# Kernel tuning notes

Measured on AMD Instinct MI355X. Metric: run time of the kernel, lower is better.

Reference implementation:

```python
import jax, jax.numpy as jnp
import numpy as np

S, L, D = 128, 512, 256   # MSA rows, residues, msa_dim
H, C = 8, 32              # num_heads, head_dim


def setup_inputs() -> dict:
    key = jax.random.key(0)
    ks = jax.random.split(key, 8)
    inp = {
        "msa_input": jax.random.normal(ks[0], (S, L, D), dtype=jnp.float32),
        "ln_scale": jnp.ones((D,), jnp.float32),
        "ln_bias": jnp.zeros((D,), jnp.float32),
        "wq": jax.random.normal(ks[1], (D, H * C), jnp.float32) / np.sqrt(D),
        "wk": jax.random.normal(ks[2], (D, H * C), jnp.float32) / np.sqrt(D),
        "wv": jax.random.normal(ks[3], (D, H * C), jnp.float32) / np.sqrt(D),
        "wg": jax.random.normal(ks[4], (D, H * C), jnp.float32) / np.sqrt(D),
        "bg": jnp.zeros((H * C,), jnp.float32),
        "wo": jax.random.normal(ks[5], (H * C, D), jnp.float32) / np.sqrt(H * C),
        "bo": jnp.zeros((D,), jnp.float32),
    }
    return inp


def reference(msa_input, ln_scale, ln_bias, wq, wk, wv, wg, bg, wo, bo):
    # LayerNorm over last dim (eps matches torch default 1e-5)
    mu = jnp.mean(msa_input, axis=-1, keepdims=True)
    var = jnp.mean(jnp.square(msa_input - mu), axis=-1, keepdims=True)
    x = (msa_input - mu) * jax.lax.rsqrt(var + 1e-5) * ln_scale + ln_bias

    q = (x @ wq).reshape(S, L, H, C)
    k = (x @ wk).reshape(S, L, H, C)
    v = (x @ wv).reshape(S, L, H, C)
    g = jax.nn.sigmoid(x @ wg + bg).reshape(S, L, H, C)

    scale = 1.0 / np.sqrt(C)
    # attention over MSA-row axis, per residue l and head h
    scores = jnp.einsum("slhc,tlhc->stlh", q, k) * scale   # [S,S,L,H]
    probs = jax.nn.softmax(scores, axis=1)                  # softmax over t
    o = jnp.einsum("stlh,tlhc->slhc", probs, v) * g         # [S,L,H,C]
    return o.reshape(S, L, H * C) @ wo + bo
```

## Files before the change

### kernel.cpp

```cpp
#include <hip/hip_runtime.h>
#include <hip/hip_bf16.h>

typedef __bf16 bf16;
typedef __bf16 bf16x8 __attribute__((ext_vector_type(8)));
typedef float f32x4 __attribute__((ext_vector_type(4)));

#define S_DIM 128
#define L_DIM 512
#define D_DIM 256
#define NQ    1024

__device__ __forceinline__ void gl16(void* lds, const void* g) {
  __builtin_amdgcn_global_load_lds((const __attribute__((address_space(1))) void*)g,
                                   (__attribute__((address_space(3))) void*)lds,
                                   16, 0, 0);
}

__global__ void pack_weights(const float* __restrict__ wq, const float* __restrict__ wk,
                             const float* __restrict__ wv, const float* __restrict__ wg,
                             const float* __restrict__ wo,
                             bf16* __restrict__ wcat_t, bf16* __restrict__ wo_t) {
  int idx = blockIdx.x * 256 + threadIdx.x;
  const int total1 = NQ * D_DIM;
  if (idx < total1) {
    int j = idx >> 8;
    int d = idx & 255;
    const float* w = (j < 256) ? wq : (j < 512) ? wk : (j < 768) ? wv : wg;
    wcat_t[idx] = (bf16)w[d * 256 + (j & 255)];
  } else {
    int i2 = idx - total1;
    if (i2 < D_DIM * D_DIM) {
      int dcol = i2 >> 8, k = i2 & 255;
      wo_t[i2] = (bf16)wo[k * 256 + dcol];
    }
  }
}

__global__ __launch_bounds__(256) void ln_kernel(const float* __restrict__ x,
                                                 const float* __restrict__ sc,
                                                 const float* __restrict__ bs,
                                                 bf16* __restrict__ y) {
  int wid  = threadIdx.x >> 6;
  int lane = threadIdx.x & 63;
  int row  = blockIdx.x * 4 + wid;
  float4 v = ((const float4*)(x + (size_t)row * D_DIM))[lane];
  float s = v.x + v.y + v.z + v.w;
  #pragma unroll
  for (int m = 32; m; m >>= 1) s += __shfl_xor(s, m);
  float mu = s * (1.0f / 256.0f);
  float dx = v.x - mu, dy = v.y - mu, dz = v.z - mu, dw = v.w - mu;
  float s2 = dx * dx + dy * dy + dz * dz + dw * dw;
  #pragma unroll
  for (int m = 32; m; m >>= 1) s2 += __shfl_xor(s2, m);
  float rs = rsqrtf(s2 * (1.0f / 256.0f) + 1e-5f);
  float4 scv = ((const float4*)sc)[lane];
  float4 bsv = ((const float4*)bs)[lane];
  union { uint2 u; bf16 b[4]; } o;
  o.b[0] = (bf16)(dx * rs * scv.x + bsv.x);
  o.b[1] = (bf16)(dy * rs * scv.y + bsv.y);
  o.b[2] = (bf16)(dz * rs * scv.z + bsv.z);
  o.b[3] = (bf16)(dw * rs * scv.w + bsv.w);
  ((uint2*)y)[(size_t)row * 64 + lane] = o.u;
}

__device__ __forceinline__ bf16x8 lds_swz(const bf16* base, int row, int k) {
  return *(const bf16x8*)((const char*)base + ((((row << 6) + k) << 1) ^ ((row & 7) << 4)));
}

__global__ __launch_bounds__(256, 4) void gemm_qkvg(const bf16* __restrict__ A,
                                                    const bf16* __restrict__ Bt,
                                                    bf16* __restrict__ Cout,
                                                    const float* __restrict__ bias) {
  __shared__ __align__(16) bf16 smem[16384];
  bf16* As = smem;
  bf16* Bs = smem + 8192;
  const int tid  = threadIdx.x;
  const int wid  = tid >> 6;
  const int lane = tid & 63;
  const int bid   = blockIdx.x;
  const int n_idx = (bid >> 3) & 7;
  const int m_idx = (bid & 7) | ((bid >> 6) << 3);
  const int m0 = m_idx * 128;
  const int n0 = n_idx * 128;
  const int lrow = lane & 15;
  const int lk   = (lane >> 4) * 8;
  const int wr = wid >> 1, wc = wid & 1;

  const int ln8 = lane >> 3;
  const int c8  = ((lane & 7) ^ ln8) * 8;

  const bf16* Arow = A  + (size_t)m0 * 256 + c8;
  const bf16* Brow = Bt + (size_t)n0 * 256 + c8;

  f32x4 acc[4][4] = {};

  #pragma unroll
  for (int ks = 0; ks < 4; ++ks) {
    const int k0 = ks * 64;
    #pragma unroll
    for (int t = 0; t < 4; ++t) {
      int chunk = wid * 4 + t;
      int r = chunk * 8 + ln8;
      gl16(&As[chunk * 512], Arow + (size_t)r * 256 + k0);
      gl16(&Bs[chunk * 512], Brow + (size_t)r * 256 + k0);
    }
    __syncthreads();
    #pragma unroll
    for (int kk = 0; kk < 64; kk += 32) {
      bf16x8 av[4], bv[4];
      #pragma unroll
      for (int i = 0; i < 4; ++i)
        av[i] = lds_swz(As, wr * 64 + i * 16 + lrow, kk + lk);
      #pragma unroll
      for (int j = 0; j < 4; ++j)
        bv[j] = lds_swz(Bs, wc * 64 + j * 16 + lrow, kk + lk);
      #pragma unroll
      for (int i = 0; i < 4; ++i)
        #pragma unroll
        for (int j = 0; j < 4; ++j)
          acc[i][j] = __builtin_amdgcn_mfma_f32_16x16x32_bf16(av[i], bv[j], acc[i][j], 0, 0, 0);
    }
    __syncthreads();
  }

  const int rb = (lane >> 4) * 4;
  const int xorv = rb << 2;

  const bool isg = (n0 >= 768);
  float bgv[4];
  if (isg) {
    #pragma unroll
    for (int j = 0; j < 4; ++j) bgv[j] = bias[n0 - 768 + wc * 64 + j * 16 + lrow];
  }
  #pragma unroll
  for (int i = 0; i < 4; ++i)
    #pragma unroll
    for (int j = 0; j < 4; ++j) {
      int col = wc * 64 + j * 16 + lrow;
      #pragma unroll
      for (int r = 0; r < 4; ++r) {
        int row = wr * 64 + i * 16 + rb + r;
        float v = acc[i][j][r];
        if (isg) { v += bgv[j]; v = 1.0f / (1.0f + __expf(-v)); }
        smem[row * 128 + (col ^ xorv)] = (bf16)v;
      }
    }
  __syncthreads();
  #pragma unroll
  for (int p = 0; p < 8; ++p) {
    int chunk = p * 256 + tid;
    int row = chunk >> 4, slot8 = (chunk & 15) * 8;
    int rx = (row & 12) << 2;
    *(uint4*)(Cout + (size_t)(m0 + row) * NQ + n0 + slot8) =
        *(const uint4*)(smem + row * 128 + (slot8 ^ rx));
  }
}

__global__ __launch_bounds__(512) void attn_proj(const bf16* __restrict__ qkvg,
                                                 const bf16* __restrict__ wo_t,
                                                 const float* __restrict__ bo,
                                                 float* __restrict__ out) {
  __shared__ __align__(16) char smem[155648];
  const int tid  = threadIdx.x;
  const int wid  = tid >> 6;
  const int lane = tid & 63;
  const int lrow = lane & 15;
  const int lkg  = lane >> 4;
  const int lk   = lkg * 8;
  const int rb   = lkg * 4;
  const int res  = blockIdx.x;
  const int hc0  = wid * 32;

  bf16* vw = (bf16*)smem + wid * (32 * 136);
  bf16* pw = (bf16*)(smem + 69632) + wid * (16 * 72);
  bf16* of = (bf16*)(smem + 88064);

  {
    int t0 = lane >> 2, cs = (lane & 3) * 8;
    #pragma unroll
    for (int pass = 0; pass < 8; ++pass) {
      int t = pass * 16 + t0;
      union { uint4 u; bf16 e[8]; } v;
      v.u = *(const uint4*)(qkvg + (size_t)(t * L_DIM + res) * NQ + 512 + hc0 + cs);
      #pragma unroll
      for (int j = 0; j < 8; ++j) vw[(cs + j) * 136 + t] = v.e[j];
    }
  }

  bf16x8 kf[8];
  #pragma unroll
  for (int tt = 0; tt < 8; ++tt)
    kf[tt] = *(const bf16x8*)(qkvg + (size_t)((tt * 16 + lrow) * L_DIM + res) * NQ + 256 + hc0 + lk);

  const float scale = 0.17677669529663687f;
  const f32x4 z = {0.f, 0.f, 0.f, 0.f};

  for (int st = 0; st < 8; ++st) {
    bf16x8 qf = *(const bf16x8*)(qkvg + (size_t)((st * 16 + lrow) * L_DIM + res) * NQ + hc0 + lk);
    f32x4 sc[8];
    #pragma unroll
    for (int tt = 0; tt < 8; ++tt)
      sc[tt] = __builtin_amdgcn_mfma_f32_16x16x32_bf16(qf, kf[tt], z, 0, 0, 0);

    #pragma unroll
    for (int r = 0; r < 4; ++r) {
      float m = sc[0][r];
      #pragma unroll
      for (int tc = 1; tc < 8; ++tc) m = fmaxf(m, sc[tc][r]);
      #pragma unroll
      for (int msk = 8; msk; msk >>= 1) m = fmaxf(m, __shfl_xor(m, msk));
      float pv[8], ssum = 0.f;
      #pragma unroll
      for (int tc = 0; tc < 8; ++tc) {
        float p = __expf((sc[tc][r] - m) * scale);
        pv[tc] = p; ssum += p;
      }
      #pragma unroll
      for (int msk = 8; msk; msk >>= 1) ssum += __shfl_xor(ssum, msk);
      float inv = 1.0f / ssum;
      #pragma unroll
      for (int tc = 0; tc < 8; ++tc) sc[tc][r] = pv[tc] * inv;
    }

    f32x4 oc[2] = {z, z};
    #pragma unroll
    for (int hf = 0; hf < 2; ++hf) {
      #pragma unroll
      for (int tc = 0; tc < 4; ++tc)
        #pragma unroll
        for (int r = 0; r < 4; ++r)
          pw[(rb + r) * 72 + tc * 16 + lrow] = (bf16)sc[hf * 4 + tc][r];
      #pragma unroll
      for (int kc = 0; kc < 2; ++kc) {
        bf16x8 pa = *(const bf16x8*)(pw + lrow * 72 + kc * 32 + lk);
        #pragma unroll
        for (int ct = 0; ct < 2; ++ct) {
          bf16x8 bv = *(const bf16x8*)(vw + (ct * 16 + lrow) * 136 + hf * 64 + kc * 32 + lk);
          oc[ct] = __builtin_amdgcn_mfma_f32_16x16x32_bf16(pa, bv, oc[ct], 0, 0, 0);
        }
      }
    }
    #pragma unroll
    for (int ct = 0; ct < 2; ++ct)
      #pragma unroll
      for (int r = 0; r < 4; ++r)
        of[(st * 16 + rb + r) * 264 + hc0 + ct * 16 + lrow] = (bf16)oc[ct][r];
  }
  __syncthreads();

  const int pbase = (wid >> 1) * 32;
  const int pn    = wid & 1;

  bf16x8 af[2][8];
  #pragma unroll
  for (int mt = 0; mt < 2; ++mt) {
    int s = pbase + mt * 16 + lrow;
    #pragma unroll
    for (int kt = 0; kt < 8; ++kt) {
      bf16x8 o8 = *(const bf16x8*)(of + s * 264 + kt * 32 + lk);
      bf16x8 g8 = *(const bf16x8*)(qkvg + (size_t)(s * L_DIM + res) * NQ + 768 + kt * 32 + lk);
      bf16x8 rr;
      #pragma unroll
      for (int j = 0; j < 8; ++j) rr[j] = (bf16)((float)o8[j] * (float)g8[j]);
      af[mt][kt] = rr;
    }
  }

  float bov[2][4];
  #pragma unroll
  for (int hf = 0; hf < 2; ++hf)
    #pragma unroll
    for (int nt = 0; nt < 4; ++nt)
      bov[hf][nt] = bo[hf * 128 + pn * 64 + nt * 16 + lrow];

  bf16* wS = (bf16*)smem;
  f32x4 acc[2][2][4] = {};
  #pragma unroll
  for (int hf = 0; hf < 2; ++hf) {
    #pragma unroll
    for (int pass = 0; pass < 8; ++pass) {
      int ch = pass * 512 + tid;
      int dl = ch >> 5, sl = ch & 31;
      gl16((char*)wS + (pass * 512 + wid * 64) * 16,
           wo_t + (size_t)(hf * 128 + dl) * 256 + (sl ^ (dl & 7)) * 8);
    }
    __syncthreads();
    #pragma unroll
    for (int kt = 0; kt < 8; ++kt)
      #pragma unroll
      for (int nt = 0; nt < 4; ++nt) {
        int dl = pn * 64 + nt * 16 + lrow;
        bf16x8 bw = *(const bf16x8*)((char*)wS + dl * 512 + (((kt * 4 + lkg) ^ (dl & 7)) * 16));
        acc[hf][0][nt] = __builtin_amdgcn_mfma_f32_16x16x32_bf16(af[0][kt], bw, acc[hf][0][nt], 0, 0, 0);
        acc[hf][1][nt] = __builtin_amdgcn_mfma_f32_16x16x32_bf16(af[1][kt], bw, acc[hf][1][nt], 0, 0, 0);
      }
    __syncthreads();
  }

  float* fb = (float*)smem;
  #pragma unroll 1
  for (int b = 0; b < 4; ++b) {
    if ((wid >> 1) == b) {
      #pragma unroll
      for (int hf = 0; hf < 2; ++hf)
        #pragma unroll
        for (int mt = 0; mt < 2; ++mt)
          #pragma unroll
          for (int nt = 0; nt < 4; ++nt)
            #pragma unroll
            for (int r = 0; r < 4; ++r)
              fb[(mt * 16 + rb + r) * 264 + hf * 128 + pn * 64 + nt * 16 + lrow] =
                  acc[hf][mt][nt][r] + bov[hf][nt];
    }
    __syncthreads();
    #pragma unroll
    for (int u = 0; u < 4; ++u) {
      int ch = u * 512 + tid;
      int row = ch >> 6, c4 = (ch & 63) * 4;
      *(uint4*)(out + (size_t)((b * 32 + row) * L_DIM + res) * 256 + c4) =
          *(const uint4*)(fb + row * 264 + c4);
    }
    __syncthreads();
  }
}

extern "C" void kernel_launch(void* const* d_in, const int* in_sizes, int n_in,
                              void* d_out, int out_size, void* d_ws, size_t ws_size,
                              hipStream_t stream) {
  const float* msa      = (const float*)d_in[0];
  const float* ln_scale = (const float*)d_in[1];
  const float* ln_bias  = (const float*)d_in[2];
  const float* wq       = (const float*)d_in[3];
  const float* wk       = (const float*)d_in[4];
  const float* wv       = (const float*)d_in[5];
  const float* wg       = (const float*)d_in[6];
  const float* bg       = (const float*)d_in[7];
  const float* wo       = (const float*)d_in[8];
  const float* bo       = (const float*)d_in[9];
  float* out = (float*)d_out;

  char* ws = (char*)d_ws;
  bf16* wcat_t = (bf16*)ws;
  bf16* wo_t   = (bf16*)(ws + 524288);
  bf16* qkvg   = (bf16*)(ws + 655360);
  bf16* x_ln   = (bf16*)d_out;

  pack_weights<<<dim3(1280), dim3(256), 0, stream>>>(wq, wk, wv, wg, wo, wcat_t, wo_t);
  ln_kernel<<<dim3(65536 / 4), dim3(256), 0, stream>>>(msa, ln_scale, ln_bias, x_ln);
  gemm_qkvg<<<dim3(4096), dim3(256), 0, stream>>>(x_ln, wcat_t, qkvg, bg);
  attn_proj<<<dim3(512), dim3(512), 0, stream>>>(qkvg, wo_t, bo, out);
}
```

Measured before the change: 156.9 us.

## Repack QKVG into per-residue head-pair panels and split attention from output projection

The QKVG GEMM now writes its output as contiguous per-(type, residue, head-pair) panels, so the attention loads are contiguous instead of strided by L*NQ. The fused attention+projection kernel becomes two kernels: a smaller attention kernel (256 threads, two blocks per residue, gating applied in-loop) that writes a bf16 gated output buffer, and a separate tiled GEMM for the output projection. This is meant to fix uncoalesced attention loads and the large-LDS, low-occupancy fused kernel. The cost is an extra global round-trip of the gated output and one more launch.

New measurement: 156.1 us. About the same (-0.5%).

```diff
diff --git a/kernel.cpp b/kernel.cpp
--- a/kernel.cpp
+++ b/kernel.cpp
@@ -69,7 +69,7 @@
 
 __global__ __launch_bounds__(256, 4) void gemm_qkvg(const bf16* __restrict__ A,
                                                     const bf16* __restrict__ Bt,
-                                                    bf16* __restrict__ Cout,
+                                                    bf16* __restrict__ pan,
                                                     const float* __restrict__ bias) {
   __shared__ __align__(16) bf16 smem[16384];
   bf16* As = smem;
@@ -126,11 +126,11 @@
   const int rb = (lane >> 4) * 4;
   const int xorv = rb << 2;
 
-  const bool isg = (n0 >= 768);
+  const bool isg = (n_idx >= 6);
   float bgv[4];
   if (isg) {
     #pragma unroll
-    for (int j = 0; j < 4; ++j) bgv[j] = bias[n0 - 768 + wc * 64 + j * 16 + lrow];
+    for (int j = 0; j < 4; ++j) bgv[j] = bias[(n_idx & 1) * 128 + wc * 64 + j * 16 + lrow];
   }
   #pragma unroll
   for (int i = 0; i < 4; ++i)
@@ -146,21 +146,24 @@
       }
     }
   __syncthreads();
+
+  const int type = n_idx >> 1;
+  const int hp0  = (n_idx & 1) * 2;
+  const int s    = m_idx >> 2;
+  const int res0 = (m_idx & 3) * 128;
   #pragma unroll
   for (int p = 0; p < 8; ++p) {
-    int chunk = p * 256 + tid;
-    int row = chunk >> 4, slot8 = (chunk & 15) * 8;
-    int rx = (row & 12) << 2;
-    *(uint4*)(Cout + (size_t)(m0 + row) * NQ + n0 + slot8) =
-        *(const uint4*)(smem + row * 128 + (slot8 ^ rx));
-  }
-}
-
-__global__ __launch_bounds__(512) void attn_proj(const bf16* __restrict__ qkvg,
-                                                 const bf16* __restrict__ wo_t,
-                                                 const float* __restrict__ bo,
-                                                 float* __restrict__ out) {
-  __shared__ __align__(16) char smem[155648];
+    int ch = p * 256 + tid;
+    int c16 = ch & 7, hpl = (ch >> 3) & 1, rr = ch >> 4;
+    int col = hpl * 64 + c16 * 8;
+    *(uint4*)(pan + ((size_t)((type * 512 + res0 + rr) * 4) + hp0 + hpl) * 8192 + s * 64 + c16 * 8) =
+        *(const uint4*)(smem + rr * 128 + (col ^ ((rr & 12) << 2)));
+  }
+}
+
+__global__ __launch_bounds__(256, 3) void attn_kernel(const bf16* __restrict__ pan,
+                                                      bf16* __restrict__ obuf) {
+  __shared__ __align__(16) char smem[48640];
   const int tid  = threadIdx.x;
   const int wid  = tid >> 6;
   const int lane = tid & 63;
@@ -168,20 +171,29 @@
   const int lkg  = lane >> 4;
   const int lk   = lkg * 8;
   const int rb   = lkg * 4;
-  const int res  = blockIdx.x;
-  const int hc0  = wid * 32;
-
-  bf16* vw = (bf16*)smem + wid * (32 * 136);
-  bf16* pw = (bf16*)(smem + 69632) + wid * (16 * 72);
-  bf16* of = (bf16*)(smem + 88064);
+  const int bid  = blockIdx.x;
+  const int res  = bid >> 1;
+  const int hg   = bid & 1;
+  const int h    = hg * 4 + wid;
+  const int hp   = h >> 1;
+  const int hl   = (h & 1) * 32;
+
+  bf16* vw  = (bf16*)smem + wid * (32 * 136);
+  bf16* pwb = (bf16*)(smem + 34816) + wid * (16 * 72);
+  bf16* osb = (bf16*)(smem + 44032) + wid * (16 * 36);
+
+  const bf16* Pq = pan + ((size_t)((0 * 512 + res) * 4) + hp) * 8192 + hl;
+  const bf16* Pk = pan + ((size_t)((1 * 512 + res) * 4) + hp) * 8192 + hl;
+  const bf16* Pv = pan + ((size_t)((2 * 512 + res) * 4) + hp) * 8192 + hl;
+  const bf16* Pg = pan + ((size_t)((3 * 512 + res) * 4) + hp) * 8192 + hl;
 
   {
     int t0 = lane >> 2, cs = (lane & 3) * 8;
     #pragma unroll
-    for (int pass = 0; pass < 8; ++pass) {
-      int t = pass * 16 + t0;
+    for (int p = 0; p < 8; ++p) {
+      int t = p * 16 + t0;
       union { uint4 u; bf16 e[8]; } v;
-      v.u = *(const uint4*)(qkvg + (size_t)(t * L_DIM + res) * NQ + 512 + hc0 + cs);
+      v.u = *(const uint4*)(Pv + t * 64 + cs);
       #pragma unroll
       for (int j = 0; j < 8; ++j) vw[(cs + j) * 136 + t] = v.e[j];
     }
@@ -190,13 +202,13 @@
   bf16x8 kf[8];
   #pragma unroll
   for (int tt = 0; tt < 8; ++tt)
-    kf[tt] = *(const bf16x8*)(qkvg + (size_t)((tt * 16 + lrow) * L_DIM + res) * NQ + 256 + hc0 + lk);
+    kf[tt] = *(const bf16x8*)(Pk + (tt * 16 + lrow) * 64 + lk);
 
   const float scale = 0.17677669529663687f;
   const f32x4 z = {0.f, 0.f, 0.f, 0.f};
 
   for (int st = 0; st < 8; ++st) {
-    bf16x8 qf = *(const bf16x8*)(qkvg + (size_t)((st * 16 + lrow) * L_DIM + res) * NQ + hc0 + lk);
+    bf16x8 qf = *(const bf16x8*)(Pq + (st * 16 + lrow) * 64 + lk);
     f32x4 sc[8];
     #pragma unroll
     for (int tt = 0; tt < 8; ++tt)
@@ -229,10 +241,10 @@
       for (int tc = 0; tc < 4; ++tc)
         #pragma unroll
         for (int r = 0; r < 4; ++r)
-          pw[(rb + r) * 72 + tc * 16 + lrow] = (bf16)sc[hf * 4 + tc][r];
+          pwb[(rb + r) * 72 + tc * 16 + lrow] = (bf16)sc[hf * 4 + tc][r];
       #pragma unroll
       for (int kc = 0; kc < 2; ++kc) {
-        bf16x8 pa = *(const bf16x8*)(pw + lrow * 72 + kc * 32 + lk);
+        bf16x8 pa = *(const bf16x8*)(pwb + lrow * 72 + kc * 32 + lk);
         #pragma unroll
         for (int ct = 0; ct < 2; ++ct) {
           bf16x8 bv = *(const bf16x8*)(vw + (ct * 16 + lrow) * 136 + hf * 64 + kc * 32 + lk);
@@ -244,83 +256,107 @@
     for (int ct = 0; ct < 2; ++ct)
       #pragma unroll
       for (int r = 0; r < 4; ++r)
-        of[(st * 16 + rb + r) * 264 + hc0 + ct * 16 + lrow] = (bf16)oc[ct][r];
-  }
-  __syncthreads();
-
-  const int pbase = (wid >> 1) * 32;
-  const int pn    = wid & 1;
-
-  bf16x8 af[2][8];
-  #pragma unroll
-  for (int mt = 0; mt < 2; ++mt) {
-    int s = pbase + mt * 16 + lrow;
-    #pragma unroll
-    for (int kt = 0; kt < 8; ++kt) {
-      bf16x8 o8 = *(const bf16x8*)(of + s * 264 + kt * 32 + lk);
-      bf16x8 g8 = *(const bf16x8*)(qkvg + (size_t)(s * L_DIM + res) * NQ + 768 + kt * 32 + lk);
-      bf16x8 rr;
-      #pragma unroll
-      for (int j = 0; j < 8; ++j) rr[j] = (bf16)((float)o8[j] * (float)g8[j]);
-      af[mt][kt] = rr;
-    }
-  }
-
-  float bov[2][4];
-  #pragma unroll
-  for (int hf = 0; hf < 2; ++hf)
-    #pragma unroll
-    for (int nt = 0; nt < 4; ++nt)
-      bov[hf][nt] = bo[hf * 128 + pn * 64 + nt * 16 + lrow];
-
-  bf16* wS = (bf16*)smem;
-  f32x4 acc[2][2][4] = {};
-  #pragma unroll
-  for (int hf = 0; hf < 2; ++hf) {
-    #pragma unroll
-    for (int pass = 0; pass < 8; ++pass) {
-      int ch = pass * 512 + tid;
-      int dl = ch >> 5, sl = ch & 31;
-      gl16((char*)wS + (pass * 512 + wid * 64) * 16,
-           wo_t + (size_t)(hf * 128 + dl) * 256 + (sl ^ (dl & 7)) * 8);
-    }
-    __syncthreads();
-    #pragma unroll
-    for (int kt = 0; kt < 8; ++kt)
-      #pragma unroll
-      for (int nt = 0; nt < 4; ++nt) {
-        int dl = pn * 64 + nt * 16 + lrow;
-        bf16x8 bw = *(const bf16x8*)((char*)wS + dl * 512 + (((kt * 4 + lkg) ^ (dl & 7)) * 16));
-        acc[hf][0][nt] = __builtin_amdgcn_mfma_f32_16x16x32_bf16(af[0][kt], bw, acc[hf][0][nt], 0, 0, 0);
-        acc[hf][1][nt] = __builtin_amdgcn_mfma_f32_16x16x32_bf16(af[1][kt], bw, acc[hf][1][nt], 0, 0, 0);
+        osb[(rb + r) * 36 + ct * 16 + lrow] = (bf16)oc[ct][r];
+    {
+      int row = lane >> 2, c16 = (lane & 3) * 8;
+      bf16x8 o8 = *(const bf16x8*)(osb + row * 36 + c16);
+      bf16x8 g8 = *(const bf16x8*)(Pg + (st * 16 + row) * 64 + c16);
+      bf16x8 r8;
+      #pragma unroll
+      for (int u = 0; u < 8; ++u) r8[u] = (bf16)((float)o8[u] * (float)g8[u]);
+      *(uint4*)(obuf + ((size_t)res * 128 + st * 16 + row) * 256 + h * 32 + c16) = *(uint4*)&r8;
+    }
+  }
+}
+
+__global__ __launch_bounds__(256, 4) void gemm_proj(const bf16* __restrict__ A,
+                                                    const bf16* __restrict__ Bt,
+                                                    float* __restrict__ Cout,
+                                                    const float* __restrict__ bias) {
+  __shared__ __align__(16) bf16 smem[16384];
+  bf16* As = smem;
+  bf16* Bs = smem + 8192;
+  const int tid  = threadIdx.x;
+  const int wid  = tid >> 6;
+  const int lane = tid & 63;
+  const int bid   = blockIdx.x;
+  const int n_idx = (bid >> 3) & 1;
+  const int m_idx = (bid & 7) | ((bid >> 4) << 3);
+  const int m0 = m_idx * 128;
+  const int n0 = n_idx * 128;
+  const int lrow = lane & 15;
+  const int lk   = (lane >> 4) * 8;
+  const int wr = wid >> 1, wc = wid & 1;
+
+  const int ln8 = lane >> 3;
+  const int c8  = ((lane & 7) ^ ln8) * 8;
+
+  const bf16* Arow = A  + (size_t)m0 * 256 + c8;
+  const bf16* Brow = Bt + (size_t)n0 * 256 + c8;
+
+  f32x4 acc[4][4] = {};
+
+  #pragma unroll
+  for (int ks = 0; ks < 4; ++ks) {
+    const int k0 = ks * 64;
+    #pragma unroll
+    for (int t = 0; t < 4; ++t) {
+      int chunk = wid * 4 + t;
+      int r = chunk * 8 + ln8;
+      gl16(&As[chunk * 512], Arow + (size_t)r * 256 + k0);
+      gl16(&Bs[chunk * 512], Brow + (size_t)r * 256 + k0);
+    }
+    __syncthreads();
+    #pragma unroll
+    for (int kk = 0; kk < 64; kk += 32) {
+      bf16x8 av[4], bv[4];
+      #pragma unroll
+      for (int i = 0; i < 4; ++i)
+        av[i] = lds_swz(As, wr * 64 + i * 16 + lrow, kk + lk);
+      #pragma unroll
+      for (int j = 0; j < 4; ++j)
+        bv[j] = lds_swz(Bs, wc * 64 + j * 16 + lrow, kk + lk);
+      #pragma unroll
+      for (int i = 0; i < 4; ++i)
+        #pragma unroll
+        for (int j = 0; j < 4; ++j)
+          acc[i][j] = __builtin_amdgcn_mfma_f32_16x16x32_bf16(av[i], bv[j], acc[i][j], 0, 0, 0);
+    }
+    __syncthreads();
+  }
+
+  const int rb = (lane >> 4) * 4;
+  const int xorv = rb << 2;
+  float* smf = (float*)smem;
+  float bov[4];
+  #pragma unroll
+  for (int j = 0; j < 4; ++j) bov[j] = bias[n0 + wc * 64 + j * 16 + lrow];
+  #pragma unroll
+  for (int half = 0; half < 2; ++half) {
+    if (half) __syncthreads();
+    #pragma unroll
+    for (int i2 = 0; i2 < 2; ++i2) {
+      int i = half * 2 + i2;
+      #pragma unroll
+      for (int j = 0; j < 4; ++j) {
+        int col = wc * 64 + j * 16 + lrow;
+        #pragma unroll
+        for (int r = 0; r < 4; ++r) {
+          int crow = wr * 32 + i2 * 16 + rb + r;
+          smf[crow * 128 + (col ^ xorv)] = acc[i][j][r] + bov[j];
+        }
       }
-    __syncthreads();
-  }
-
-  float* fb = (float*)smem;
-  #pragma unroll 1
-  for (int b = 0; b < 4; ++b) {
-    if ((wid >> 1) == b) {
-      #pragma unroll
-      for (int hf = 0; hf < 2; ++hf)
-        #pragma unroll
-        for (int mt = 0; mt < 2; ++mt)
-          #pragma unroll
-          for (int nt = 0; nt < 4; ++nt)
-            #pragma unroll
-            for (int r = 0; r < 4; ++r)
-              fb[(mt * 16 + rb + r) * 264 + hf * 128 + pn * 64 + nt * 16 + lrow] =
-                  acc[hf][mt][nt][r] + bov[hf][nt];
-    }
-    __syncthreads();
-    #pragma unroll
-    for (int u = 0; u < 4; ++u) {
-      int ch = u * 512 + tid;
-      int row = ch >> 6, c4 = (ch & 63) * 4;
-      *(uint4*)(out + (size_t)((b * 32 + row) * L_DIM + res) * 256 + c4) =
-          *(const uint4*)(fb + row * 264 + c4);
-    }
-    __syncthreads();
+    }
+    __syncthreads();
+    #pragma unroll
+    for (int p = 0; p < 8; ++p) {
+      int ch = p * 256 + tid;
+      int crow = ch >> 5, slot = (ch & 31) * 4;
+      int rx = (crow & 12) << 2;
+      int s_loc = (crow >> 5) * 64 + half * 32 + (crow & 31);
+      *(uint4*)(Cout + ((size_t)s_loc * 512 + m_idx) * 256 + n0 + slot) =
+          *(const uint4*)(smf + crow * 128 + (slot ^ rx));
+    }
   }
 }
 
@@ -342,11 +378,13 @@
   char* ws = (char*)d_ws;
   bf16* wcat_t = (bf16*)ws;
   bf16* wo_t   = (bf16*)(ws + 524288);
-  bf16* qkvg   = (bf16*)(ws + 655360);
+  bf16* pan    = (bf16*)(ws + 655360);
+  bf16* obuf   = (bf16*)(ws + 655360 + 134217728ULL);
   bf16* x_ln   = (bf16*)d_out;
 
   pack_weights<<<dim3(1280), dim3(256), 0, stream>>>(wq, wk, wv, wg, wo, wcat_t, wo_t);
   ln_kernel<<<dim3(65536 / 4), dim3(256), 0, stream>>>(msa, ln_scale, ln_bias, x_ln);
-  gemm_qkvg<<<dim3(4096), dim3(256), 0, stream>>>(x_ln, wcat_t, qkvg, bg);
-  attn_proj<<<dim3(512), dim3(512), 0, stream>>>(qkvg, wo_t, bo, out);
-}
+  gemm_qkvg<<<dim3(4096), dim3(256), 0, stream>>>(x_ln, wcat_t, pan, bg);
+  attn_kernel<<<dim3(1024), dim3(256), 0, stream>>>(pan, obuf);
+  gemm_proj<<<dim3(1024), dim3(256), 0, stream>>>(obuf, wo_t, out, bo);
+}
```

## Fuse LayerNorm into QKVG projection per residue and write head-panel layout

Applied to the files above, without the earlier changes.

Merges the LayerNorm and QKVG GEMM kernels into one per-residue kernel. It normalizes all 128 MSA rows into LDS, streams the concatenated weights in double-buffered 64-column chunks, and writes Q/K/V/G into a per-residue, per-head-pair panel layout. The attention kernel then reads contiguous panels instead of rows strided by L. This removes the bf16 LN round trip through global memory and one launch. In exchange it uses only 512 blocks with large LDS, and each block re-reads the full weight matrix.

After: 154.2 us. About the same (-1.7%).

```diff
diff --git a/kernel.cpp b/kernel.cpp
--- a/kernel.cpp
+++ b/kernel.cpp
@@ -36,130 +36,147 @@
   }
 }
 
-__global__ __launch_bounds__(256) void ln_kernel(const float* __restrict__ x,
-                                                 const float* __restrict__ sc,
-                                                 const float* __restrict__ bs,
-                                                 bf16* __restrict__ y) {
-  int wid  = threadIdx.x >> 6;
-  int lane = threadIdx.x & 63;
-  int row  = blockIdx.x * 4 + wid;
-  float4 v = ((const float4*)(x + (size_t)row * D_DIM))[lane];
-  float s = v.x + v.y + v.z + v.w;
-  #pragma unroll
-  for (int m = 32; m; m >>= 1) s += __shfl_xor(s, m);
-  float mu = s * (1.0f / 256.0f);
-  float dx = v.x - mu, dy = v.y - mu, dz = v.z - mu, dw = v.w - mu;
-  float s2 = dx * dx + dy * dy + dz * dz + dw * dw;
-  #pragma unroll
-  for (int m = 32; m; m >>= 1) s2 += __shfl_xor(s2, m);
-  float rs = rsqrtf(s2 * (1.0f / 256.0f) + 1e-5f);
-  float4 scv = ((const float4*)sc)[lane];
-  float4 bsv = ((const float4*)bs)[lane];
-  union { uint2 u; bf16 b[4]; } o;
-  o.b[0] = (bf16)(dx * rs * scv.x + bsv.x);
-  o.b[1] = (bf16)(dy * rs * scv.y + bsv.y);
-  o.b[2] = (bf16)(dz * rs * scv.z + bsv.z);
-  o.b[3] = (bf16)(dw * rs * scv.w + bsv.w);
-  ((uint2*)y)[(size_t)row * 64 + lane] = o.u;
-}
-
-__device__ __forceinline__ bf16x8 lds_swz(const bf16* base, int row, int k) {
-  return *(const bf16x8*)((const char*)base + ((((row << 6) + k) << 1) ^ ((row & 7) << 4)));
-}
-
-__global__ __launch_bounds__(256, 4) void gemm_qkvg(const bf16* __restrict__ A,
-                                                    const bf16* __restrict__ Bt,
-                                                    bf16* __restrict__ Cout,
-                                                    const float* __restrict__ bias) {
-  __shared__ __align__(16) bf16 smem[16384];
-  bf16* As = smem;
-  bf16* Bs = smem + 8192;
+__global__ __launch_bounds__(512, 2) void ln_qkvg(const float* __restrict__ msa,
+                                                  const float* __restrict__ lns,
+                                                  const float* __restrict__ lnb,
+                                                  const bf16* __restrict__ wcat,
+                                                  const float* __restrict__ bg,
+                                                  bf16* __restrict__ pan) {
+  __shared__ __align__(16) char smem[147456];
+  bf16* Albs = (bf16*)smem;
+  char* Bb   = smem + 65536;
+  bf16* Cst  = (bf16*)(smem + 131072);
   const int tid  = threadIdx.x;
   const int wid  = tid >> 6;
   const int lane = tid & 63;
-  const int bid   = blockIdx.x;
-  const int n_idx = (bid >> 3) & 7;
-  const int m_idx = (bid & 7) | ((bid >> 6) << 3);
-  const int m0 = m_idx * 128;
-  const int n0 = n_idx * 128;
   const int lrow = lane & 15;
-  const int lk   = (lane >> 4) * 8;
-  const int wr = wid >> 1, wc = wid & 1;
-
-  const int ln8 = lane >> 3;
-  const int c8  = ((lane & 7) ^ ln8) * 8;
-
-  const bf16* Arow = A  + (size_t)m0 * 256 + c8;
-  const bf16* Brow = Bt + (size_t)n0 * 256 + c8;
-
-  f32x4 acc[4][4] = {};
-
-  #pragma unroll
-  for (int ks = 0; ks < 4; ++ks) {
-    const int k0 = ks * 64;
-    #pragma unroll
-    for (int t = 0; t < 4; ++t) {
-      int chunk = wid * 4 + t;
-      int r = chunk * 8 + ln8;
-      gl16(&As[chunk * 512], Arow + (size_t)r * 256 + k0);
-      gl16(&Bs[chunk * 512], Brow + (size_t)r * 256 + k0);
-    }
-    __syncthreads();
-    #pragma unroll
-    for (int kk = 0; kk < 64; kk += 32) {
-      bf16x8 av[4], bv[4];
+  const int lkg  = lane >> 4;
+  const int lk   = lkg * 8;
+  const int rb   = lkg * 4;
+  const int res  = blockIdx.x;
+
+  #pragma unroll
+  for (int p = 0; p < 4; ++p) {
+    int ch = p * 512 + tid;
+    int n = ch >> 5;
+    int inner = (ch & 31) * 16;
+    gl16(Bb + p * 8192 + wid * 1024,
+         (const char*)wcat + (size_t)n * 512 + (inner ^ ((n & 7) << 4)));
+  }
+
+  {
+    float4 scv = ((const float4*)lns)[lane];
+    float4 bsv = ((const float4*)lnb)[lane];
+    const float* mbase = msa + ((size_t)(wid * 16) * 512 + res) * 256 + lane * 4;
+    #pragma unroll
+    for (int b4 = 0; b4 < 4; ++b4) {
+      float4 rv[4];
       #pragma unroll
       for (int i = 0; i < 4; ++i)
-        av[i] = lds_swz(As, wr * 64 + i * 16 + lrow, kk + lk);
-      #pragma unroll
-      for (int j = 0; j < 4; ++j)
-        bv[j] = lds_swz(Bs, wc * 64 + j * 16 + lrow, kk + lk);
-      #pragma unroll
-      for (int i = 0; i < 4; ++i)
-        #pragma unroll
-        for (int j = 0; j < 4; ++j)
-          acc[i][j] = __builtin_amdgcn_mfma_f32_16x16x32_bf16(av[i], bv[j], acc[i][j], 0, 0, 0);
-    }
-    __syncthreads();
-  }
-
-  const int rb = (lane >> 4) * 4;
-  const int xorv = rb << 2;
-
-  const bool isg = (n0 >= 768);
-  float bgv[4];
-  if (isg) {
-    #pragma unroll
-    for (int j = 0; j < 4; ++j) bgv[j] = bias[n0 - 768 + wc * 64 + j * 16 + lrow];
-  }
-  #pragma unroll
-  for (int i = 0; i < 4; ++i)
-    #pragma unroll
-    for (int j = 0; j < 4; ++j) {
-      int col = wc * 64 + j * 16 + lrow;
-      #pragma unroll
-      for (int r = 0; r < 4; ++r) {
-        int row = wr * 64 + i * 16 + rb + r;
-        float v = acc[i][j][r];
-        if (isg) { v += bgv[j]; v = 1.0f / (1.0f + __expf(-v)); }
-        smem[row * 128 + (col ^ xorv)] = (bf16)v;
-      }
-    }
+        rv[i] = *(const float4*)(mbase + (size_t)(b4 * 4 + i) * 512 * 256);
+      #pragma unroll
+      for (int i = 0; i < 4; ++i) {
+        int s = wid * 16 + b4 * 4 + i;
+        float4 v = rv[i];
+        float sum = v.x + v.y + v.z + v.w;
+        #pragma unroll
+        for (int m = 32; m; m >>= 1) sum += __shfl_xor(sum, m);
+        float mu = sum * (1.0f / 256.0f);
+        float dx = v.x - mu, dy = v.y - mu, dz = v.z - mu, dw = v.w - mu;
+        float s2 = dx * dx + dy * dy + dz * dz + dw * dw;
+        #pragma unroll
+        for (int m = 32; m; m >>= 1) s2 += __shfl_xor(s2, m);
+        float rs = rsqrtf(s2 * (1.0f / 256.0f) + 1e-5f);
+        union { uint2 u; bf16 b[4]; } o;
+        o.b[0] = (bf16)(dx * rs * scv.x + bsv.x);
+        o.b[1] = (bf16)(dy * rs * scv.y + bsv.y);
+        o.b[2] = (bf16)(dz * rs * scv.z + bsv.z);
+        o.b[3] = (bf16)(dw * rs * scv.w + bsv.w);
+        *(uint2*)((char*)Albs + (((s * 512) + lane * 8) ^ ((s & 7) << 4))) = o.u;
+      }
+    }
+  }
   __syncthreads();
-  #pragma unroll
-  for (int p = 0; p < 8; ++p) {
-    int chunk = p * 256 + tid;
-    int row = chunk >> 4, slot8 = (chunk & 15) * 8;
-    int rx = (row & 12) << 2;
-    *(uint4*)(Cout + (size_t)(m0 + row) * NQ + n0 + slot8) =
-        *(const uint4*)(smem + row * 128 + (slot8 ^ rx));
-  }
-}
-
-__global__ __launch_bounds__(512) void attn_proj(const bf16* __restrict__ qkvg,
-                                                 const bf16* __restrict__ wo_t,
-                                                 const float* __restrict__ bo,
-                                                 float* __restrict__ out) {
+
+  const int mq = wid & 3;
+  const int nh = wid >> 2;
+
+  bf16x8 afc[2][8];
+  #pragma unroll
+  for (int mt = 0; mt < 2; ++mt)
+    #pragma unroll
+    for (int kk = 0; kk < 8; ++kk) {
+      int row = mq * 32 + mt * 16 + lrow;
+      afc[mt][kk] = *(const bf16x8*)((char*)Albs +
+                      (((row * 512) + (kk * 32 + lk) * 2) ^ ((row & 7) << 4)));
+    }
+
+  for (int cc = 0; cc < 16; ++cc) {
+    char* Bcur = Bb + (cc & 1) * 32768;
+    if (cc < 15) {
+      char* Bnxt = Bb + ((cc + 1) & 1) * 32768;
+      const size_t ncol0 = (size_t)(cc + 1) * 64;
+      #pragma unroll
+      for (int p = 0; p < 4; ++p) {
+        int ch = p * 512 + tid;
+        int n = ch >> 5;
+        int inner = (ch & 31) * 16;
+        gl16(Bnxt + p * 8192 + wid * 1024,
+             (const char*)wcat + (ncol0 + n) * 512 + (inner ^ ((n & 7) << 4)));
+      }
+    }
+    f32x4 acc[2][2] = {};
+    #pragma unroll
+    for (int kk = 0; kk < 8; ++kk) {
+      bf16x8 bv[2];
+      #pragma unroll
+      for (int nt = 0; nt < 2; ++nt) {
+        int nl = nh * 32 + nt * 16 + lrow;
+        bv[nt] = *(const bf16x8*)(Bcur +
+                    (((nl * 512) + (kk * 32 + lk) * 2) ^ ((nl & 7) << 4)));
+      }
+      #pragma unroll
+      for (int mt = 0; mt < 2; ++mt)
+        #pragma unroll
+        for (int nt = 0; nt < 2; ++nt)
+          acc[mt][nt] = __builtin_amdgcn_mfma_f32_16x16x32_bf16(afc[mt][kk], bv[nt], acc[mt][nt], 0, 0, 0);
+    }
+    const bool isg = (cc >= 12);
+    #pragma unroll
+    for (int mt = 0; mt < 2; ++mt)
+      #pragma unroll
+      for (int nt = 0; nt < 2; ++nt) {
+        int col = nh * 32 + nt * 16 + lrow;
+        float bgv = isg ? bg[(cc - 12) * 64 + col] : 0.f;
+        #pragma unroll
+        for (int r = 0; r < 4; ++r) {
+          int row = mq * 32 + mt * 16 + rb + r;
+          float v = acc[mt][nt][r];
+          if (isg) { v += bgv; v = 1.0f / (1.0f + __expf(-v)); }
+          Cst[row * 64 + (col ^ (rb << 2))] = (bf16)v;
+        }
+      }
+    __syncthreads();
+    {
+      const int type = cc >> 2, hp = cc & 3;
+      bf16* pbase = pan + ((size_t)((type * 512 + res) * 4) + hp) * 8192;
+      #pragma unroll
+      for (int p = 0; p < 2; ++p) {
+        int ch = p * 512 + tid;
+        int rr = ch >> 3, c16 = ch & 7;
+        *(uint4*)(pbase + rr * 64 + c16 * 8) =
+            *(const uint4*)(Cst + rr * 64 + ((c16 * 8) ^ ((rr & 12) << 2)));
+      }
+    }
+    asm volatile("s_waitcnt lgkmcnt(0)" ::: "memory");
+    __builtin_amdgcn_s_barrier();
+  }
+}
+
+__global__ __launch_bounds__(512, 2) void attn_proj(const bf16* __restrict__ pan,
+                                                    const bf16* __restrict__ wo_t,
+                                                    const float* __restrict__ bo,
+                                                    float* __restrict__ out) {
   __shared__ __align__(16) char smem[155648];
   const int tid  = threadIdx.x;
   const int wid  = tid >> 6;
@@ -169,19 +186,25 @@
   const int lk   = lkg * 8;
   const int rb   = lkg * 4;
   const int res  = blockIdx.x;
-  const int hc0  = wid * 32;
-
-  bf16* vw = (bf16*)smem + wid * (32 * 136);
-  bf16* pw = (bf16*)(smem + 69632) + wid * (16 * 72);
-  bf16* of = (bf16*)(smem + 88064);
+  const int h    = wid;
+  const int hp   = h >> 1;
+  const int hl   = (h & 1) * 32;
+
+  bf16* vw  = (bf16*)(smem + wid * 8704);
+  bf16* pwb = (bf16*)(smem + 69632 + wid * 2304);
+  bf16* of  = (bf16*)(smem + 88064);
+
+  const bf16* Pq = pan + ((size_t)((0 * 512 + res) * 4) + hp) * 8192 + hl;
+  const bf16* Pk = pan + ((size_t)((1 * 512 + res) * 4) + hp) * 8192 + hl;
+  const bf16* Pv = pan + ((size_t)((2 * 512 + res) * 4) + hp) * 8192 + hl;
 
   {
     int t0 = lane >> 2, cs = (lane & 3) * 8;
     #pragma unroll
-    for (int pass = 0; pass < 8; ++pass) {
-      int t = pass * 16 + t0;
+    for (int p = 0; p < 8; ++p) {
+      int t = p * 16 + t0;
       union { uint4 u; bf16 e[8]; } v;
-      v.u = *(const uint4*)(qkvg + (size_t)(t * L_DIM + res) * NQ + 512 + hc0 + cs);
+      v.u = *(const uint4*)(Pv + t * 64 + cs);
       #pragma unroll
       for (int j = 0; j < 8; ++j) vw[(cs + j) * 136 + t] = v.e[j];
     }
@@ -190,13 +213,13 @@
   bf16x8 kf[8];
   #pragma unroll
   for (int tt = 0; tt < 8; ++tt)
-    kf[tt] = *(const bf16x8*)(qkvg + (size_t)((tt * 16 + lrow) * L_DIM + res) * NQ + 256 + hc0 + lk);
+    kf[tt] = *(const bf16x8*)(Pk + (tt * 16 + lrow) * 64 + lk);
 
   const float scale = 0.17677669529663687f;
   const f32x4 z = {0.f, 0.f, 0.f, 0.f};
 
   for (int st = 0; st < 8; ++st) {
-    bf16x8 qf = *(const bf16x8*)(qkvg + (size_t)((st * 16 + lrow) * L_DIM + res) * NQ + hc0 + lk);
+    bf16x8 qf = *(const bf16x8*)(Pq + (st * 16 + lrow) * 64 + lk);
     f32x4 sc[8];
     #pragma unroll
     for (int tt = 0; tt < 8; ++tt)
@@ -229,10 +252,10 @@
       for (int tc = 0; tc < 4; ++tc)
         #pragma unroll
         for (int r = 0; r < 4; ++r)
-          pw[(rb + r) * 72 + tc * 16 + lrow] = (bf16)sc[hf * 4 + tc][r];
+          pwb[(rb + r) * 72 + tc * 16 + lrow] = (bf16)sc[hf * 4 + tc][r];
       #pragma unroll
       for (int kc = 0; kc < 2; ++kc) {
-        bf16x8 pa = *(const bf16x8*)(pw + lrow * 72 + kc * 32 + lk);
+        bf16x8 pa = *(const bf16x8*)(pwb + lrow * 72 + kc * 32 + lk);
         #pragma unroll
         for (int ct = 0; ct < 2; ++ct) {
           bf16x8 bv = *(const bf16x8*)(vw + (ct * 16 + lrow) * 136 + hf * 64 + kc * 32 + lk);
@@ -244,21 +267,22 @@
     for (int ct = 0; ct < 2; ++ct)
       #pragma unroll
       for (int r = 0; r < 4; ++r)
-        of[(st * 16 + rb + r) * 264 + hc0 + ct * 16 + lrow] = (bf16)oc[ct][r];
+        of[(st * 16 + rb + r) * 264 + h * 32 + ct * 16 + lrow] = (bf16)oc[ct][r];
   }
   __syncthreads();
 
-  const int pbase = (wid >> 1) * 32;
-  const int pn    = wid & 1;
+  const int wm = wid >> 1;
+  const int pn = wid & 1;
 
   bf16x8 af[2][8];
   #pragma unroll
   for (int mt = 0; mt < 2; ++mt) {
-    int s = pbase + mt * 16 + lrow;
+    int s = wm * 32 + mt * 16 + lrow;
     #pragma unroll
     for (int kt = 0; kt < 8; ++kt) {
       bf16x8 o8 = *(const bf16x8*)(of + s * 264 + kt * 32 + lk);
-      bf16x8 g8 = *(const bf16x8*)(qkvg + (size_t)(s * L_DIM + res) * NQ + 768 + kt * 32 + lk);
+      bf16x8 g8 = *(const bf16x8*)(pan + ((size_t)((3 * 512 + res) * 4) + (kt >> 1)) * 8192 +
+                                   (kt & 1) * 32 + s * 64 + lk);
       bf16x8 rr;
       #pragma unroll
       for (int j = 0; j < 8; ++j) rr[j] = (bf16)((float)o8[j] * (float)g8[j]);
@@ -278,11 +302,11 @@
   #pragma unroll
   for (int hf = 0; hf < 2; ++hf) {
     #pragma unroll
-    for (int pass = 0; pass < 8; ++pass) {
-      int ch = pass * 512 + tid;
+    for (int p = 0; p < 8; ++p) {
+      int ch = p * 512 + tid;
       int dl = ch >> 5, sl = ch & 31;
-      gl16((char*)wS + (pass * 512 + wid * 64) * 16,
-           wo_t + (size_t)(hf * 128 + dl) * 256 + (sl ^ (dl & 7)) * 8);
+      gl16((char*)wS + p * 8192 + wid * 1024,
+           (const char*)wo_t + (size_t)(hf * 128 + dl) * 512 + (((sl * 16) ^ ((dl & 7) << 4))));
     }
     __syncthreads();
     #pragma unroll
@@ -290,7 +314,7 @@
       #pragma unroll
       for (int nt = 0; nt < 4; ++nt) {
         int dl = pn * 64 + nt * 16 + lrow;
-        bf16x8 bw = *(const bf16x8*)((char*)wS + dl * 512 + (((kt * 4 + lkg) ^ (dl & 7)) * 16));
+        bf16x8 bw = *(const bf16x8*)((char*)wS + dl * 512 + (((kt * 4 + lkg) ^ (dl & 7)) << 4));
         acc[hf][0][nt] = __builtin_amdgcn_mfma_f32_16x16x32_bf16(af[0][kt], bw, acc[hf][0][nt], 0, 0, 0);
         acc[hf][1][nt] = __builtin_amdgcn_mfma_f32_16x16x32_bf16(af[1][kt], bw, acc[hf][1][nt], 0, 0, 0);
       }
@@ -300,7 +324,7 @@
   float* fb = (float*)smem;
   #pragma unroll 1
   for (int b = 0; b < 4; ++b) {
-    if ((wid >> 1) == b) {
+    if (wm == b) {
       #pragma unroll
       for (int hf = 0; hf < 2; ++hf)
         #pragma unroll
@@ -317,7 +341,7 @@
     for (int u = 0; u < 4; ++u) {
       int ch = u * 512 + tid;
       int row = ch >> 6, c4 = (ch & 63) * 4;
-      *(uint4*)(out + (size_t)((b * 32 + row) * L_DIM + res) * 256 + c4) =
+      *(uint4*)(out + ((size_t)(b * 32 + row) * L_DIM + res) * 256 + c4) =
           *(const uint4*)(fb + row * 264 + c4);
     }
     __syncthreads();
@@ -342,11 +366,9 @@
   char* ws = (char*)d_ws;
   bf16* wcat_t = (bf16*)ws;
   bf16* wo_t   = (bf16*)(ws + 524288);
-  bf16* qkvg   = (bf16*)(ws + 655360);
-  bf16* x_ln   = (bf16*)d_out;
+  bf16* pan    = (bf16*)(ws + 655360);
 
   pack_weights<<<dim3(1280), dim3(256), 0, stream>>>(wq, wk, wv, wg, wo, wcat_t, wo_t);
-  ln_kernel<<<dim3(65536 / 4), dim3(256), 0, stream>>>(msa, ln_scale, ln_bias, x_ln);
-  gemm_qkvg<<<dim3(4096), dim3(256), 0, stream>>>(x_ln, wcat_t, qkvg, bg);
-  attn_proj<<<dim3(512), dim3(512), 0, stream>>>(qkvg, wo_t, bo, out);
-}
+  ln_qkvg<<<dim3(512), dim3(512), 0, stream>>>(msa, ln_scale, ln_bias, wcat_t, bg, pan);
+  attn_proj<<<dim3(512), dim3(512), 0, stream>>>(pan, wo_t, bo, out);
+}
```

## Store QKVG projections in per-residue head-pair panels for contiguous attention loads

Applied to the files above, without the earlier changes.

The QKVG GEMM epilogue now scatters its output into a panel layout indexed by type, residue and head pair, with the 128 MSA rows stored contiguously at 64 elements each. The attention kernel then reads Q, K, V and gate tiles for one residue from small contiguous regions instead of from rows strided by L*1024. The goal is fewer scattered global reads and better cache-line use in attn_proj. In exchange, the GEMM epilogue writes are less contiguous, and a launch-bounds occupancy hint of 2 blocks is added even though each block uses about 152 KB of LDS.

After: 157.3 us. Within noise of the previous version (+0.2%).

```diff
diff --git a/kernel.cpp b/kernel.cpp
--- a/kernel.cpp
+++ b/kernel.cpp
@@ -69,7 +69,7 @@
 
 __global__ __launch_bounds__(256, 4) void gemm_qkvg(const bf16* __restrict__ A,
                                                     const bf16* __restrict__ Bt,
-                                                    bf16* __restrict__ Cout,
+                                                    bf16* __restrict__ pan,
                                                     const float* __restrict__ bias) {
   __shared__ __align__(16) bf16 smem[16384];
   bf16* As = smem;
@@ -126,11 +126,11 @@
   const int rb = (lane >> 4) * 4;
   const int xorv = rb << 2;
 
-  const bool isg = (n0 >= 768);
+  const bool isg = (n_idx >= 6);
   float bgv[4];
   if (isg) {
     #pragma unroll
-    for (int j = 0; j < 4; ++j) bgv[j] = bias[n0 - 768 + wc * 64 + j * 16 + lrow];
+    for (int j = 0; j < 4; ++j) bgv[j] = bias[(n_idx & 1) * 128 + wc * 64 + j * 16 + lrow];
   }
   #pragma unroll
   for (int i = 0; i < 4; ++i)
@@ -146,20 +146,25 @@
       }
     }
   __syncthreads();
+
+  const int type = n_idx >> 1;
+  const int hp0  = (n_idx & 1) * 2;
+  const int s    = m_idx >> 2;
+  const int res0 = (m_idx & 3) * 128;
   #pragma unroll
   for (int p = 0; p < 8; ++p) {
-    int chunk = p * 256 + tid;
-    int row = chunk >> 4, slot8 = (chunk & 15) * 8;
-    int rx = (row & 12) << 2;
-    *(uint4*)(Cout + (size_t)(m0 + row) * NQ + n0 + slot8) =
-        *(const uint4*)(smem + row * 128 + (slot8 ^ rx));
-  }
-}
-
-__global__ __launch_bounds__(512) void attn_proj(const bf16* __restrict__ qkvg,
-                                                 const bf16* __restrict__ wo_t,
-                                                 const float* __restrict__ bo,
-                                                 float* __restrict__ out) {
+    int ch = p * 256 + tid;
+    int c16 = ch & 7, hpl = (ch >> 3) & 1, rr = ch >> 4;
+    int col = hpl * 64 + c16 * 8;
+    *(uint4*)(pan + ((size_t)((type * 512 + res0 + rr) * 4) + hp0 + hpl) * 8192 + s * 64 + c16 * 8) =
+        *(const uint4*)(smem + rr * 128 + (col ^ ((rr & 12) << 2)));
+  }
+}
+
+__global__ __launch_bounds__(512, 2) void attn_proj(const bf16* __restrict__ pan,
+                                                    const bf16* __restrict__ wo_t,
+                                                    const float* __restrict__ bo,
+                                                    float* __restrict__ out) {
   __shared__ __align__(16) char smem[155648];
   const int tid  = threadIdx.x;
   const int wid  = tid >> 6;
@@ -169,19 +174,25 @@
   const int lk   = lkg * 8;
   const int rb   = lkg * 4;
   const int res  = blockIdx.x;
-  const int hc0  = wid * 32;
-
-  bf16* vw = (bf16*)smem + wid * (32 * 136);
-  bf16* pw = (bf16*)(smem + 69632) + wid * (16 * 72);
-  bf16* of = (bf16*)(smem + 88064);
+  const int h    = wid;
+  const int hp   = h >> 1;
+  const int hl   = (h & 1) * 32;
+
+  bf16* vw  = (bf16*)(smem + wid * 8704);
+  bf16* pwb = (bf16*)(smem + 69632 + wid * 2304);
+  bf16* of  = (bf16*)(smem + 88064);
+
+  const bf16* Pq = pan + ((size_t)((0 * 512 + res) * 4) + hp) * 8192 + hl;
+  const bf16* Pk = pan + ((size_t)((1 * 512 + res) * 4) + hp) * 8192 + hl;
+  const bf16* Pv = pan + ((size_t)((2 * 512 + res) * 4) + hp) * 8192 + hl;
 
   {
     int t0 = lane >> 2, cs = (lane & 3) * 8;
     #pragma unroll
-    for (int pass = 0; pass < 8; ++pass) {
-      int t = pass * 16 + t0;
+    for (int p = 0; p < 8; ++p) {
+      int t = p * 16 + t0;
       union { uint4 u; bf16 e[8]; } v;
-      v.u = *(const uint4*)(qkvg + (size_t)(t * L_DIM + res) * NQ + 512 + hc0 + cs);
+      v.u = *(const uint4*)(Pv + t * 64 + cs);
       #pragma unroll
       for (int j = 0; j < 8; ++j) vw[(cs + j) * 136 + t] = v.e[j];
     }
@@ -190,13 +201,13 @@
   bf16x8 kf[8];
   #pragma unroll
   for (int tt = 0; tt < 8; ++tt)
-    kf[tt] = *(const bf16x8*)(qkvg + (size_t)((tt * 16 + lrow) * L_DIM + res) * NQ + 256 + hc0 + lk);
+    kf[tt] = *(const bf16x8*)(Pk + (tt * 16 + lrow) * 64 + lk);
 
   const float scale = 0.17677669529663687f;
   const f32x4 z = {0.f, 0.f, 0.f, 0.f};
 
   for (int st = 0; st < 8; ++st) {
-    bf16x8 qf = *(const bf16x8*)(qkvg + (size_t)((st * 16 + lrow) * L_DIM + res) * NQ + hc0 + lk);
+    bf16x8 qf = *(const bf16x8*)(Pq + (st * 16 + lrow) * 64 + lk);
     f32x4 sc[8];
     #pragma unroll
     for (int tt = 0; tt < 8; ++tt)
@@ -229,10 +240,10 @@
       for (int tc = 0; tc < 4; ++tc)
         #pragma unroll
         for (int r = 0; r < 4; ++r)
-          pw[(rb + r) * 72 + tc * 16 + lrow] = (bf16)sc[hf * 4 + tc][r];
+          pwb[(rb + r) * 72 + tc * 16 + lrow] = (bf16)sc[hf * 4 + tc][r];
       #pragma unroll
       for (int kc = 0; kc < 2; ++kc) {
-        bf16x8 pa = *(const bf16x8*)(pw + lrow * 72 + kc * 32 + lk);
+        bf16x8 pa = *(const bf16x8*)(pwb + lrow * 72 + kc * 32 + lk);
         #pragma unroll
         for (int ct = 0; ct < 2; ++ct) {
           bf16x8 bv = *(const bf16x8*)(vw + (ct * 16 + lrow) * 136 + hf * 64 + kc * 32 + lk);
@@ -244,21 +255,22 @@
     for (int ct = 0; ct < 2; ++ct)
       #pragma unroll
       for (int r = 0; r < 4; ++r)
-        of[(st * 16 + rb + r) * 264 + hc0 + ct * 16 + lrow] = (bf16)oc[ct][r];
+        of[(st * 16 + rb + r) * 264 + h * 32 + ct * 16 + lrow] = (bf16)oc[ct][r];
   }
   __syncthreads();
 
-  const int pbase = (wid >> 1) * 32;
-  const int pn    = wid & 1;
+  const int wm = wid >> 1;
+  const int pn = wid & 1;
 
   bf16x8 af[2][8];
   #pragma unroll
   for (int mt = 0; mt < 2; ++mt) {
-    int s = pbase + mt * 16 + lrow;
+    int s = wm * 32 + mt * 16 + lrow;
     #pragma unroll
     for (int kt = 0; kt < 8; ++kt) {
       bf16x8 o8 = *(const bf16x8*)(of + s * 264 + kt * 32 + lk);
-      bf16x8 g8 = *(const bf16x8*)(qkvg + (size_t)(s * L_DIM + res) * NQ + 768 + kt * 32 + lk);
+      bf16x8 g8 = *(const bf16x8*)(pan + ((size_t)((3 * 512 + res) * 4) + (kt >> 1)) * 8192 +
+                                   (kt & 1) * 32 + s * 64 + lk);
       bf16x8 rr;
       #pragma unroll
       for (int j = 0; j < 8; ++j) rr[j] = (bf16)((float)o8[j] * (float)g8[j]);
@@ -278,11 +290,11 @@
   #pragma unroll
   for (int hf = 0; hf < 2; ++hf) {
     #pragma unroll
-    for (int pass = 0; pass < 8; ++pass) {
-      int ch = pass * 512 + tid;
+    for (int p = 0; p < 8; ++p) {
+      int ch = p * 512 + tid;
       int dl = ch >> 5, sl = ch & 31;
-      gl16((char*)wS + (pass * 512 + wid * 64) * 16,
-           wo_t + (size_t)(hf * 128 + dl) * 256 + (sl ^ (dl & 7)) * 8);
+      gl16((char*)wS + p * 8192 + wid * 1024,
+           (const char*)wo_t + (size_t)(hf * 128 + dl) * 512 + (((sl * 16) ^ ((dl & 7) << 4))));
     }
     __syncthreads();
     #pragma unroll
@@ -290,7 +302,7 @@
       #pragma unroll
       for (int nt = 0; nt < 4; ++nt) {
         int dl = pn * 64 + nt * 16 + lrow;
-        bf16x8 bw = *(const bf16x8*)((char*)wS + dl * 512 + (((kt * 4 + lkg) ^ (dl & 7)) * 16));
+        bf16x8 bw = *(const bf16x8*)((char*)wS + dl * 512 + (((kt * 4 + lkg) ^ (dl & 7)) << 4));
         acc[hf][0][nt] = __builtin_amdgcn_mfma_f32_16x16x32_bf16(af[0][kt], bw, acc[hf][0][nt], 0, 0, 0);
         acc[hf][1][nt] = __builtin_amdgcn_mfma_f32_16x16x32_bf16(af[1][kt], bw, acc[hf][1][nt], 0, 0, 0);
       }
@@ -300,7 +312,7 @@
   float* fb = (float*)smem;
   #pragma unroll 1
   for (int b = 0; b < 4; ++b) {
-    if ((wid >> 1) == b) {
+    if (wm == b) {
       #pragma unroll
       for (int hf = 0; hf < 2; ++hf)
         #pragma unroll
@@ -317,7 +329,7 @@
     for (int u = 0; u < 4; ++u) {
       int ch = u * 512 + tid;
       int row = ch >> 6, c4 = (ch & 63) * 4;
-      *(uint4*)(out + (size_t)((b * 32 + row) * L_DIM + res) * 256 + c4) =
+      *(uint4*)(out + ((size_t)(b * 32 + row) * L_DIM + res) * 256 + c4) =
           *(const uint4*)(fb + row * 264 + c4);
     }
     __syncthreads();
@@ -342,11 +354,11 @@
   char* ws = (char*)d_ws;
   bf16* wcat_t = (bf16*)ws;
   bf16* wo_t   = (bf16*)(ws + 524288);
-  bf16* qkvg   = (bf16*)(ws + 655360);
+  bf16* pan    = (bf16*)(ws + 655360);
   bf16* x_ln   = (bf16*)d_out;
 
   pack_weights<<<dim3(1280), dim3(256), 0, stream>>>(wq, wk, wv, wg, wo, wcat_t, wo_t);
   ln_kernel<<<dim3(65536 / 4), dim3(256), 0, stream>>>(msa, ln_scale, ln_bias, x_ln);
-  gemm_qkvg<<<dim3(4096), dim3(256), 0, stream>>>(x_ln, wcat_t, qkvg, bg);
-  attn_proj<<<dim3(512), dim3(512), 0, stream>>>(qkvg, wo_t, bo, out);
-}
+  gemm_qkvg<<<dim3(4096), dim3(256), 0, stream>>>(x_ln, wcat_t, pan, bg);
+  attn_proj<<<dim3(512), dim3(512), 0, stream>>>(pan, wo_t, bo, out);
+}
```
